# Optimization experiments

Hardware: AMD Instinct MI355X
Metric: run time of the kernel (lower is better)

The kernel has to match this reference:

```python
import jax, jax.numpy as jnp
import numpy as np

VEC, HID, B, S = 1280, 128, 4, 256
EPS = 1e-5


def _ln(x):
    m = x.mean(-1, keepdims=True)
    v = ((x - m) ** 2).mean(-1, keepdims=True)
    return (x - m) / jnp.sqrt(v + EPS)


def _add_attn(q_in, kv_in, Wq, Wk, wv):
    # Additive (Bahdanau) attention: scores[b,i,j] = wv . tanh(q[b,i] + k[b,j])
    q = q_in @ Wq            # [B, Sq, H]
    k = kv_in @ Wk           # [B, Sk, H]
    feat = jnp.tanh(q[:, :, None, :] + k[:, None, :, :])   # [B, Sq, Sk, H]
    scores = jnp.einsum('bijh,h->bij', feat, wv)
    attn = jax.nn.softmax(scores, axis=-1)
    return jnp.einsum('bij,bjd->bid', attn, kv_in)          # values = kv_in


def _res_fc(x, W1, b1, W2, b2):
    return jnp.maximum(x @ W1 + b1, 0.0) @ W2 + b2 + x


def setup_inputs() -> dict:
    key = jax.random.key(0)
    ks = iter(jax.random.split(key, 64))
    d = {
        'X': jax.random.normal(next(ks), (B, S, VEC), dtype=jnp.float32),
        'lys_pos': 100,
    }
    sc = 0.02
    for i in (1, 2, 3, 4):
        d[f'Wq{i}'] = jax.random.normal(next(ks), (VEC, HID), dtype=jnp.float32) * sc
        d[f'Wk{i}'] = jax.random.normal(next(ks), (VEC, HID), dtype=jnp.float32) * sc
        d[f'wv{i}'] = jax.random.normal(next(ks), (HID,), dtype=jnp.float32) * sc
    for i in (1, 2, 3):
        d[f'rW1_{i}'] = jax.random.normal(next(ks), (VEC, HID), dtype=jnp.float32) * sc
        d[f'rb1_{i}'] = jnp.zeros((HID,), dtype=jnp.float32)
        d[f'rW2_{i}'] = jax.random.normal(next(ks), (HID, VEC), dtype=jnp.float32) * sc
        d[f'rb2_{i}'] = jnp.zeros((VEC,), dtype=jnp.float32)
    d['hW1'] = jax.random.normal(next(ks), (VEC, 32), dtype=jnp.float32) * sc
    d['hb1'] = jnp.zeros((32,), dtype=jnp.float32)
    d['hW2'] = jax.random.normal(next(ks), (32, 12), dtype=jnp.float32) * sc
    d['hb2'] = jnp.zeros((12,), dtype=jnp.float32)
    d['hW3'] = jax.random.normal(next(ks), (12, 2), dtype=jnp.float32) * sc
    d['hb3'] = jnp.zeros((2,), dtype=jnp.float32)
    return d


def reference(X, lys_pos,
              Wq1, Wk1, wv1, Wq2, Wk2, wv2, Wq3, Wk3, wv3, Wq4, Wk4, wv4,
              rW1_1, rb1_1, rW2_1, rb2_1,
              rW1_2, rb1_2, rW2_2, rb2_2,
              rW1_3, rb1_3, rW2_3, rb2_3,
              hW1, hb1, hW2, hb2, hW3, hb3):
    X = X.astype(jnp.float32)
    X = _ln(_add_attn(X, X, Wq1, Wk1, wv1) + X)
    X = _res_fc(X, rW1_1, rb1_1, rW2_1, rb2_1)
    X = _ln(_add_attn(X, X, Wq2, Wk2, wv2) + X)
    X = _res_fc(X, rW1_2, rb1_2, rW2_2, rb2_2)
    X = _ln(_add_attn(X, X, Wq3, Wk3, wv3) + X)
    X = _res_fc(X, rW1_3, rb1_3, rW2_3, rb2_3)
    X_lys = X[:, lys_pos, :][:, None, :]                    # [B, 1, VEC]
    X_lys = _ln(_add_attn(X_lys, X, Wq4, Wk4, wv4) + X_lys)
    h = jnp.maximum(X_lys @ hW1 + hb1, 0.0)                 # dropout = identity (eval)
    h = jnp.maximum(h @ hW2 + hb2, 0.0)
    logits = (h @ hW3 + hb3)[:, 0, :]                       # squeeze(1) -> [B, 2]
    return logits
```

## Files before the change

kernel.cpp:

```cpp
#include <hip/hip_runtime.h>


#define DEV __device__ __forceinline__

static constexpr int VEC = 1280;
static constexpr int HID = 128;
static constexpr int BB  = 4;
static constexpr int SS  = 256;
static constexpr int MROWS = BB * SS;
static constexpr int NPART = 8;

DEV float ftanh(float x) {
  float e = __expf(2.0f * x);
  return 1.0f - __fdividef(2.0f, e + 1.0f);
}

DEV float waveSum(float v) {
#pragma unroll
  for (int off = 32; off > 0; off >>= 1) v += __shfl_xor(v, off, 64);
  return v;
}
DEV float waveMax(float v) {
#pragma unroll
  for (int off = 32; off > 0; off >>= 1) v = fmaxf(v, __shfl_xor(v, off, 64));
  return v;
}
DEV float blockSum(float v, float* red) {
  v = waveSum(v);
  int tid = threadIdx.x;
  if ((tid & 63) == 0) red[tid >> 6] = v;
  __syncthreads();
  float r = (red[0] + red[1]) + (red[2] + red[3]);
  __syncthreads();
  return r;
}
DEV float blockMax(float v, float* red) {
  v = waveMax(v);
  int tid = threadIdx.x;
  if ((tid & 63) == 0) red[tid >> 6] = v;
  __syncthreads();
  float r = fmaxf(fmaxf(red[0], red[1]), fmaxf(red[2], red[3]));
  __syncthreads();
  return r;
}

template <int MODE, bool AFUSE, bool OBIAS, bool ORES>
__global__ __launch_bounds__(256) void gemm_k(
    const float* __restrict__ A, long sAb, long aPart,
    const float* __restrict__ B0, const float* __restrict__ B1, int nSplitB,
    long sBb, int ldB,
    float* __restrict__ C, long sCb,
    const float* __restrict__ aBias, const float* __restrict__ oBias,
    const float* __restrict__ res,
    int N, int K, int kChunk) {
  const int n0 = blockIdx.x * 64;
  const int m0 = blockIdx.y * 64;
  const int z  = blockIdx.z;

  const float* Ab = A + (MODE == 2 ? (long)z * sAb : 0L);
  float*       Cb = C + (MODE >= 1 ? (long)z * sCb : 0L);
  const float* resz = ORES ? (res + (MODE == 2 ? (long)z * sCb : 0L)) : nullptr;
  const float* Bsel;
  int nb;
  if (n0 < nSplitB) { Bsel = B0; nb = n0; } else { Bsel = B1; nb = n0 - nSplitB; }
  if (MODE == 2) Bsel += (long)z * sBb;

  const int kBeg = (MODE == 1) ? z * kChunk : 0;
  const int kEnd = (MODE == 1) ? kBeg + kChunk : K;

  __shared__ float As[16][68];
  __shared__ float Bs[16][68];

  const int tid = threadIdx.x;
  const int tx = tid & 15, ty = tid >> 4;
  const int ar = tid >> 2, ac = (tid & 3) << 2;
  const int br = tid >> 4, bc = (tid & 15) << 2;

  auto loadA = [&](int kt) -> float4 {
    const size_t aoff = (size_t)(m0 + ar) * K + kt + ac;
    if (AFUSE) {
      float4 s = *(const float4*)(Ab + aoff);
#pragma unroll
      for (int p = 1; p < NPART; ++p) {
        const float4 t = *(const float4*)(Ab + (long)p * aPart + aoff);
        s.x += t.x; s.y += t.y; s.z += t.z; s.w += t.w;
      }
      const float4 bz = *(const float4*)(aBias + kt + ac);
      s.x = fmaxf(s.x + bz.x, 0.0f);
      s.y = fmaxf(s.y + bz.y, 0.0f);
      s.z = fmaxf(s.z + bz.z, 0.0f);
      s.w = fmaxf(s.w + bz.w, 0.0f);
      return s;
    }
    return *(const float4*)(Ab + aoff);
  };
  auto loadB = [&](int kt) -> float4 {
    return *(const float4*)(Bsel + (size_t)(kt + br) * ldB + nb + bc);
  };

  float acc[4][4] = {};
  float4 a4 = loadA(kBeg);
  float4 b4 = loadB(kBeg);

  for (int kt = kBeg; kt < kEnd; kt += 16) {
    __syncthreads();
    As[ac + 0][ar] = a4.x;
    As[ac + 1][ar] = a4.y;
    As[ac + 2][ar] = a4.z;
    As[ac + 3][ar] = a4.w;
    *(float4*)&Bs[br][bc] = b4;
    __syncthreads();
    if (kt + 16 < kEnd) {
      a4 = loadA(kt + 16);
      b4 = loadB(kt + 16);
    }
#pragma unroll
    for (int kk = 0; kk < 16; ++kk) {
      const float4 av = *(const float4*)&As[kk][ty << 2];
      const float4 bv = *(const float4*)&Bs[kk][tx << 2];
      const float a[4] = {av.x, av.y, av.z, av.w};
      const float b[4] = {bv.x, bv.y, bv.z, bv.w};
#pragma unroll
      for (int i = 0; i < 4; ++i)
#pragma unroll
        for (int j = 0; j < 4; ++j) acc[i][j] = fmaf(a[i], b[j], acc[i][j]);
    }
  }

#pragma unroll
  for (int i = 0; i < 4; ++i) {
    const int m = m0 + (ty << 2) + i;
#pragma unroll
    for (int j = 0; j < 4; ++j) {
      const int n = n0 + (tx << 2) + j;
      float v = acc[i][j];
      if (OBIAS) v += oBias[n];
      if (ORES) v += resz[(size_t)m * N + n];
      Cb[(size_t)m * N + n] = v;
    }
  }
}

__global__ __launch_bounds__(256) void qksum_k(const float* __restrict__ QKp,
                                               long ps,
                                               float* __restrict__ Qd,
                                               float* __restrict__ KT) {
  const int r = blockIdx.x, tid = threadIdx.x;
  const int b = r >> 8, j = r & 255;
  const size_t off = (size_t)r * 256 + tid;
  float v = 0.0f;
#pragma unroll
  for (int p = 0; p < NPART; ++p) v += QKp[(long)p * ps + off];
  if (tid < 128) {
    Qd[(size_t)r * 128 + tid] = v;
  } else {
    KT[(size_t)b * 32768 + (size_t)(tid - 128) * 256 + j] = v;
  }
}

__global__ __launch_bounds__(256) void scores2_k(const float* __restrict__ Qd,
                                                 const float* __restrict__ KT,
                                                 const float* __restrict__ wv,
                                                 float* __restrict__ attn) {
  const int b = blockIdx.y, i0 = blockIdx.x * 2, tid = threadIdx.x;
  __shared__ float qs[2][128], wvs[128], red[4];
  {
    const int rr = tid >> 7, h = tid & 127;
    qs[rr][h] = Qd[(size_t)(b * 256 + i0 + rr) * 128 + h];
  }
  if (tid < 128) wvs[tid] = wv[tid];
  __syncthreads();

  const float* KTb = KT + (size_t)b * 32768 + tid;
  float s0 = 0.0f, s1 = 0.0f;
#pragma unroll 4
  for (int h = 0; h < 128; h += 4) {
    const float k0 = KTb[(h + 0) * 256];
    const float k1 = KTb[(h + 1) * 256];
    const float k2 = KTb[(h + 2) * 256];
    const float k3 = KTb[(h + 3) * 256];
    const float w0 = wvs[h], w1 = wvs[h + 1], w2 = wvs[h + 2], w3 = wvs[h + 3];
    s0 += w0 * ftanh(qs[0][h] + k0) + w1 * ftanh(qs[0][h + 1] + k1) +
          w2 * ftanh(qs[0][h + 2] + k2) + w3 * ftanh(qs[0][h + 3] + k3);
    s1 += w0 * ftanh(qs[1][h] + k0) + w1 * ftanh(qs[1][h + 1] + k1) +
          w2 * ftanh(qs[1][h + 2] + k2) + w3 * ftanh(qs[1][h + 3] + k3);
  }
  {
    const float mx = blockMax(s0, red);
    const float e = __expf(s0 - mx);
    const float tot = blockSum(e, red);
    attn[(size_t)(b * 256 + i0) * 256 + tid] = e / tot;
  }
  {
    const float mx = blockMax(s1, red);
    const float e = __expf(s1 - mx);
    const float tot = blockSum(e, red);
    attn[(size_t)(b * 256 + i0 + 1) * 256 + tid] = e / tot;
  }
}

__global__ __launch_bounds__(256) void ln1_k(const float* __restrict__ A,
                                             float* __restrict__ Y) {
  __shared__ float red[4];
  const int r = blockIdx.x, tid = threadIdx.x;
  const float* a = A + (size_t)r * VEC;
  float v[5];
  float sum = 0.0f;
#pragma unroll
  for (int k = 0; k < 5; ++k) {
    v[k] = a[tid + k * 256];
    sum += v[k];
  }
  sum = blockSum(sum, red);
  const float m = sum * (1.0f / VEC);
  float sq = 0.0f;
#pragma unroll
  for (int k = 0; k < 5; ++k) {
    const float dl = v[k] - m;
    sq += dl * dl;
  }
  sq = blockSum(sq, red);
  const float rstd = rsqrtf(sq * (1.0f / VEC) + 1e-5f);
  float* y = Y + (size_t)r * VEC;
#pragma unroll
  for (int k = 0; k < 5; ++k) y[tid + k * 256] = (v[k] - m) * rstd;
}

__global__ __launch_bounds__(256) void scores4_k(const float* __restrict__ Qd,
                                                 const float* __restrict__ KT,
                                                 const float* __restrict__ wv4,
                                                 const int* __restrict__ lys,
                                                 float* __restrict__ aw4) {
  const int b = blockIdx.x, tid = threadIdx.x;
  __shared__ float qs[128], wvs[128], red[4];
  const int lp = lys[0];
  if (tid < 128) {
    qs[tid] = Qd[(size_t)(b * 256 + lp) * 128 + tid];
    wvs[tid] = wv4[tid];
  }
  __syncthreads();
  const float* KTb = KT + (size_t)b * 32768 + tid;
  float s = 0.0f;
#pragma unroll 4
  for (int h = 0; h < 128; h += 4) {
    s += wvs[h + 0] * ftanh(qs[h + 0] + KTb[(h + 0) * 256]);
    s += wvs[h + 1] * ftanh(qs[h + 1] + KTb[(h + 1) * 256]);
    s += wvs[h + 2] * ftanh(qs[h + 2] + KTb[(h + 2) * 256]);
    s += wvs[h + 3] * ftanh(qs[h + 3] + KTb[(h + 3) * 256]);
  }
  const float mx = blockMax(s, red);
  const float e = __expf(s - mx);
  const float tot = blockSum(e, red);
  aw4[b * 256 + tid] = e / tot;
}

__global__ __launch_bounds__(256) void pv4_k(const float* __restrict__ aw4,
                                             const float* __restrict__ X3,
                                             const int* __restrict__ lys,
                                             float* __restrict__ A4) {
  const int b = blockIdx.x, c = blockIdx.y * 256 + threadIdx.x;
  __shared__ float aws[256];
  aws[threadIdx.x] = aw4[b * 256 + threadIdx.x];
  __syncthreads();
  const float* Xb = X3 + (size_t)b * SS * VEC;
  float acc = 0.0f;
#pragma unroll 8
  for (int j = 0; j < 256; ++j) acc = fmaf(aws[j], Xb[(size_t)j * VEC + c], acc);
  acc += Xb[(size_t)lys[0] * VEC + c];
  A4[b * VEC + c] = acc;
}

__global__ __launch_bounds__(256) void lnhead_k(
    const float* __restrict__ A4,
    const float* __restrict__ hW1, const float* __restrict__ hb1,
    const float* __restrict__ hW2, const float* __restrict__ hb2,
    const float* __restrict__ hW3, const float* __restrict__ hb3,
    float* __restrict__ out) {
  const int b = blockIdx.x, tid = threadIdx.x;
  __shared__ float xrow[1280], partial[256], red[4];
  __shared__ float h1s[32], h2s[12];
  float v[5];
  float sum = 0.0f;
#pragma unroll
  for (int k = 0; k < 5; ++k) {
    v[k] = A4[b * VEC + tid + k * 256];
    sum += v[k];
  }
  sum = blockSum(sum, red);
  const float m = sum * (1.0f / VEC);
  float sq = 0.0f;
#pragma unroll
  for (int k = 0; k < 5; ++k) {
    const float dl = v[k] - m;
    sq += dl * dl;
  }
  sq = blockSum(sq, red);
  const float rstd = rsqrtf(sq * (1.0f / VEC) + 1e-5f);
#pragma unroll
  for (int k = 0; k < 5; ++k) xrow[tid + k * 256] = (v[k] - m) * rstd;
  __syncthreads();
  {
    const int n = tid & 31, sl = tid >> 5;
    float p = 0.0f;
    for (int k = sl * 160; k < sl * 160 + 160; ++k)
      p = fmaf(xrow[k], hW1[(size_t)k * 32 + n], p);
    partial[tid] = p;
  }
  __syncthreads();
  if (tid < 32) {
    float t = 0.0f;
#pragma unroll
    for (int s2 = 0; s2 < 8; ++s2) t += partial[s2 * 32 + tid];
    h1s[tid] = fmaxf(t + hb1[tid], 0.0f);
  }
  __syncthreads();
  if (tid < 12) {
    float t = 0.0f;
#pragma unroll
    for (int k = 0; k < 32; ++k) t = fmaf(h1s[k], hW2[k * 12 + tid], t);
    h2s[tid] = fmaxf(t + hb2[tid], 0.0f);
  }
  __syncthreads();
  if (tid < 2) {
    float t = 0.0f;
#pragma unroll
    for (int k = 0; k < 12; ++k) t = fmaf(h2s[k], hW3[k * 2 + tid], t);
    out[b * 2 + tid] = t + hb3[tid];
  }
}

extern "C" void kernel_launch(void* const* d_in, const int* in_sizes, int n_in,
                              void* d_out, int out_size, void* d_ws, size_t ws_size,
                              hipStream_t stream) {
  const float* X = (const float*)d_in[0];
  const int* lys = (const int*)d_in[1];
  const float* Wq[4] = {(const float*)d_in[2], (const float*)d_in[5],
                        (const float*)d_in[8], (const float*)d_in[11]};
  const float* Wk[4] = {(const float*)d_in[3], (const float*)d_in[6],
                        (const float*)d_in[9], (const float*)d_in[12]};
  const float* wv[4] = {(const float*)d_in[4], (const float*)d_in[7],
                        (const float*)d_in[10], (const float*)d_in[13]};
  const float* rW1[3] = {(const float*)d_in[14], (const float*)d_in[18],
                         (const float*)d_in[22]};
  const float* rb1[3] = {(const float*)d_in[15], (const float*)d_in[19],
                         (const float*)d_in[23]};
  const float* rW2[3] = {(const float*)d_in[16], (const float*)d_in[20],
                         (const float*)d_in[24]};
  const float* rb2[3] = {(const float*)d_in[17], (const float*)d_in[21],
                         (const float*)d_in[25]};
  const float* hW1 = (const float*)d_in[26];
  const float* hb1 = (const float*)d_in[27];
  const float* hW2 = (const float*)d_in[28];
  const float* hb2 = (const float*)d_in[29];
  const float* hW3 = (const float*)d_in[30];
  const float* hb3 = (const float*)d_in[31];
  float* out = (float*)d_out;

  float* ws = (float*)d_ws;
  const long QK_PS = 262144;
  const long H_PS  = 131072;
  float* QKp  = ws;
  float* Qd   = QKp + (long)NPART * QK_PS;
  float* KT   = Qd + 131072;
  float* attn = KT + 131072;
  float* Yraw = attn + 262144;
  float* Yb   = Yraw + 1310720;
  float* Hp   = Yb + 1310720;
  float* buf0 = Hp + (long)NPART * H_PS;
  float* buf1 = buf0 + 1310720;
  float* aw4  = buf1 + 1310720;
  float* A4   = aw4 + 1024;

  const int NSPLIT_NONE = 1 << 30;
  const float* P[3] = {X, buf0, buf1};
  float* Q[3] = {buf0, buf1, buf0};

  for (int l = 0; l < 3; ++l) {
    const float* Xin = P[l];
    gemm_k<1, false, false, false><<<dim3(4, 16, NPART), 256, 0, stream>>>(
        Xin, 0, 0, Wq[l], Wk[l], HID, 0, HID, QKp, QK_PS, nullptr, nullptr,
        nullptr, 256, VEC, 160);
    qksum_k<<<dim3(MROWS), 256, 0, stream>>>(QKp, QK_PS, Qd, KT);
    scores2_k<<<dim3(128, BB), 256, 0, stream>>>(Qd, KT, wv[l], attn);
    gemm_k<2, false, false, true><<<dim3(20, 4, BB), 256, 0, stream>>>(
        attn, (long)SS * SS, 0, Xin, Xin, NSPLIT_NONE, (long)SS * VEC, VEC,
        Yraw, (long)SS * VEC, nullptr, nullptr, Xin, VEC, SS, 0);
    ln1_k<<<dim3(MROWS), 256, 0, stream>>>(Yraw, Yb);
    gemm_k<1, false, false, false><<<dim3(2, 16, NPART), 256, 0, stream>>>(
        Yb, 0, 0, rW1[l], rW1[l], NSPLIT_NONE, 0, HID, Hp, H_PS, nullptr,
        nullptr, nullptr, HID, VEC, 160);
    gemm_k<0, true, true, true><<<dim3(20, 16, 1), 256, 0, stream>>>(
        Hp, 0, H_PS, rW2[l], rW2[l], NSPLIT_NONE, 0, VEC, Q[l], 0, rb1[l],
        rb2[l], Yb, VEC, HID, 0);
  }

  const float* X3 = Q[2];
  gemm_k<1, false, false, false><<<dim3(4, 16, NPART), 256, 0, stream>>>(
      X3, 0, 0, Wq[3], Wk[3], HID, 0, HID, QKp, QK_PS, nullptr, nullptr,
      nullptr, 256, VEC, 160);
  qksum_k<<<dim3(MROWS), 256, 0, stream>>>(QKp, QK_PS, Qd, KT);
  scores4_k<<<dim3(BB), 256, 0, stream>>>(Qd, KT, wv[3], lys, aw4);
  pv4_k<<<dim3(BB, 5), 256, 0, stream>>>(aw4, X3, lys, A4);
  lnhead_k<<<dim3(BB), 256, 0, stream>>>(A4, hW1, hb1, hW2, hb2, hW3, hb3, out);
}
```

Before: 445.2 us.

## Fuse whole network into one persistent cooperative kernel with grid syncs

Replaces the sequence of about 26 separate kernel launches with a single cooperative persistent kernel of 256 blocks. Each stage loops over virtual blocks and stages are separated by grid-wide syncs, removing launch overhead and inter-kernel gaps. The final attention stage is also trimmed: only K is projected for all rows, while Q is computed for just the single lys row per batch. The cost is that each stage runs on a fixed 256-block grid with one block per CU, which limits occupancy for the GEMM stages, and grid.sync adds its own barrier cost.

```diff
diff --git a/kernel.cpp b/kernel.cpp
--- a/kernel.cpp
+++ b/kernel.cpp
@@ -1,4 +1,7 @@
 #include <hip/hip_runtime.h>
+#include <hip/hip_cooperative_groups.h>
+
+namespace cg = cooperative_groups;
 
 
 #define DEV __device__ __forceinline__
@@ -44,58 +47,47 @@
   return r;
 }
 
-template <int MODE, bool AFUSE, bool OBIAS, bool ORES>
-__global__ __launch_bounds__(256) void gemm_k(
-    const float* __restrict__ A, long sAb, long aPart,
-    const float* __restrict__ B0, const float* __restrict__ B1, int nSplitB,
-    long sBb, int ldB,
-    float* __restrict__ C, long sCb,
-    const float* __restrict__ aBias, const float* __restrict__ oBias,
-    const float* __restrict__ res,
-    int N, int K, int kChunk) {
-  const int n0 = blockIdx.x * 64;
-  const int m0 = blockIdx.y * 64;
-  const int z  = blockIdx.z;
-
-  const float* Ab = A + (MODE == 2 ? (long)z * sAb : 0L);
-  float*       Cb = C + (MODE >= 1 ? (long)z * sCb : 0L);
-  const float* resz = ORES ? (res + (MODE == 2 ? (long)z * sCb : 0L)) : nullptr;
-  const float* Bsel;
-  int nb;
-  if (n0 < nSplitB) { Bsel = B0; nb = n0; } else { Bsel = B1; nb = n0 - nSplitB; }
-  if (MODE == 2) Bsel += (long)z * sBb;
-
-  const int kBeg = (MODE == 1) ? z * kChunk : 0;
-  const int kEnd = (MODE == 1) ? kBeg + kChunk : K;
-
-  __shared__ float As[16][68];
-  __shared__ float Bs[16][68];
-
+struct SmemGemm { float As[16][68]; float Bs[16][68]; };
+union Smem {
+  SmemGemm g;
+  struct { float qs[2][128]; float wvs[128]; } s;
+  struct { float xrow[1280]; float partial[256]; float h1s[32]; float h2s[12]; } t;
+  float aws[256];
+};
+
+template <int NP, bool AFUSE, bool OBIAS, bool ORES>
+DEV void gemm_tile(SmemGemm& smg,
+                   const float* __restrict__ A, int ldA, long aPart,
+                   const float* __restrict__ B, int ldB, int nb,
+                   float* __restrict__ C, int ldC,
+                   int m0, int n0, int kBeg, int kEnd,
+                   const float* __restrict__ aBias,
+                   const float* __restrict__ oBias,
+                   const float* __restrict__ res) {
   const int tid = threadIdx.x;
   const int tx = tid & 15, ty = tid >> 4;
   const int ar = tid >> 2, ac = (tid & 3) << 2;
   const int br = tid >> 4, bc = (tid & 15) << 2;
 
   auto loadA = [&](int kt) -> float4 {
-    const size_t aoff = (size_t)(m0 + ar) * K + kt + ac;
+    const size_t off = (size_t)(m0 + ar) * ldA + kt + ac;
+    float4 s = *(const float4*)(A + off);
     if (AFUSE) {
-      float4 s = *(const float4*)(Ab + aoff);
-#pragma unroll
-      for (int p = 1; p < NPART; ++p) {
-        const float4 t = *(const float4*)(Ab + (long)p * aPart + aoff);
-        s.x += t.x; s.y += t.y; s.z += t.z; s.w += t.w;
+#pragma unroll
+      for (int p2 = 1; p2 < NP; ++p2) {
+        const float4 t2 = *(const float4*)(A + (long)p2 * aPart + off);
+        s.x += t2.x; s.y += t2.y; s.z += t2.z; s.w += t2.w;
       }
       const float4 bz = *(const float4*)(aBias + kt + ac);
       s.x = fmaxf(s.x + bz.x, 0.0f);
       s.y = fmaxf(s.y + bz.y, 0.0f);
       s.z = fmaxf(s.z + bz.z, 0.0f);
       s.w = fmaxf(s.w + bz.w, 0.0f);
-      return s;
-    }
-    return *(const float4*)(Ab + aoff);
+    }
+    return s;
   };
   auto loadB = [&](int kt) -> float4 {
-    return *(const float4*)(Bsel + (size_t)(kt + br) * ldB + nb + bc);
+    return *(const float4*)(B + (size_t)(kt + br) * ldB + nb + bc);
   };
 
   float acc[4][4] = {};
@@ -104,11 +96,11 @@
 
   for (int kt = kBeg; kt < kEnd; kt += 16) {
     __syncthreads();
-    As[ac + 0][ar] = a4.x;
-    As[ac + 1][ar] = a4.y;
-    As[ac + 2][ar] = a4.z;
-    As[ac + 3][ar] = a4.w;
-    *(float4*)&Bs[br][bc] = b4;
+    smg.As[ac + 0][ar] = a4.x;
+    smg.As[ac + 1][ar] = a4.y;
+    smg.As[ac + 2][ar] = a4.z;
+    smg.As[ac + 3][ar] = a4.w;
+    *(float4*)&smg.Bs[br][bc] = b4;
     __syncthreads();
     if (kt + 16 < kEnd) {
       a4 = loadA(kt + 16);
@@ -116,8 +108,8 @@
     }
 #pragma unroll
     for (int kk = 0; kk < 16; ++kk) {
-      const float4 av = *(const float4*)&As[kk][ty << 2];
-      const float4 bv = *(const float4*)&Bs[kk][tx << 2];
+      const float4 av = *(const float4*)&smg.As[kk][ty << 2];
+      const float4 bv = *(const float4*)&smg.Bs[kk][tx << 2];
       const float a[4] = {av.x, av.y, av.z, av.w};
       const float b[4] = {bv.x, bv.y, bv.z, bv.w};
 #pragma unroll
@@ -135,271 +127,328 @@
       const int n = n0 + (tx << 2) + j;
       float v = acc[i][j];
       if (OBIAS) v += oBias[n];
-      if (ORES) v += resz[(size_t)m * N + n];
-      Cb[(size_t)m * N + n] = v;
-    }
-  }
-}
-
-__global__ __launch_bounds__(256) void qksum_k(const float* __restrict__ QKp,
-                                               long ps,
-                                               float* __restrict__ Qd,
-                                               float* __restrict__ KT) {
-  const int r = blockIdx.x, tid = threadIdx.x;
-  const int b = r >> 8, j = r & 255;
-  const size_t off = (size_t)r * 256 + tid;
-  float v = 0.0f;
-#pragma unroll
-  for (int p = 0; p < NPART; ++p) v += QKp[(long)p * ps + off];
-  if (tid < 128) {
-    Qd[(size_t)r * 128 + tid] = v;
-  } else {
-    KT[(size_t)b * 32768 + (size_t)(tid - 128) * 256 + j] = v;
-  }
-}
-
-__global__ __launch_bounds__(256) void scores2_k(const float* __restrict__ Qd,
-                                                 const float* __restrict__ KT,
-                                                 const float* __restrict__ wv,
-                                                 float* __restrict__ attn) {
-  const int b = blockIdx.y, i0 = blockIdx.x * 2, tid = threadIdx.x;
-  __shared__ float qs[2][128], wvs[128], red[4];
-  {
-    const int rr = tid >> 7, h = tid & 127;
-    qs[rr][h] = Qd[(size_t)(b * 256 + i0 + rr) * 128 + h];
-  }
-  if (tid < 128) wvs[tid] = wv[tid];
-  __syncthreads();
-
-  const float* KTb = KT + (size_t)b * 32768 + tid;
-  float s0 = 0.0f, s1 = 0.0f;
+      if (ORES) v += res[(size_t)m * ldC + n];
+      C[(size_t)m * ldC + n] = v;
+    }
+  }
+}
+
+struct Params {
+  const float* X; const int* lys;
+  const float* Wq[4]; const float* Wk[4]; const float* wv[4];
+  const float* rW1[3]; const float* rb1[3];
+  const float* rW2[3]; const float* rb2[3];
+  const float* hW1; const float* hb1;
+  const float* hW2; const float* hb2;
+  const float* hW3; const float* hb3;
+  float* out;
+  float* QKp; float* Qd; float* KT; float* attn;
+  float* Yraw; float* Yb; float* Hp;
+  float* buf0; float* buf1;
+  float* q4d; float* aw4; float* A4;
+};
+
+static constexpr long QK_PS = 262144;
+static constexpr long H_PS  = 131072;
+
+__global__ __launch_bounds__(256, 1) void net_k(Params p) {
+  cg::grid_group grid = cg::this_grid();
+  __shared__ Smem sm;
+  __shared__ float red[4];
+  const int blk = blockIdx.x, G = gridDim.x, tid = threadIdx.x;
+
+  const float* Pin[3] = {p.X, p.buf0, p.buf1};
+  float* Pout[3] = {p.buf0, p.buf1, p.buf0};
+
+  for (int l = 0; l < 3; ++l) {
+    const float* Xin = Pin[l];
+
+    for (int vb = blk; vb < 512; vb += G) {
+      const int x = vb & 3, y = (vb >> 2) & 15, z = vb >> 6;
+      const int n0 = x * 64;
+      const float* Bsel = (n0 < HID) ? p.Wq[l] : p.Wk[l];
+      const int nb = (n0 < HID) ? n0 : n0 - HID;
+      gemm_tile<1, false, false, false>(
+          sm.g, Xin, VEC, 0, Bsel, HID, nb, p.QKp + (long)z * QK_PS, 256,
+          y * 64, n0, z * 160, z * 160 + 160, nullptr, nullptr, nullptr);
+    }
+    grid.sync();
+
+    for (int vb = blk; vb < MROWS; vb += G) {
+      const int b = vb >> 8, j = vb & 255;
+      const size_t off = (size_t)vb * 256 + tid;
+      float v = 0.0f;
+#pragma unroll
+      for (int q = 0; q < NPART; ++q) v += p.QKp[(long)q * QK_PS + off];
+      if (tid < 128) p.Qd[(size_t)vb * 128 + tid] = v;
+      else p.KT[(size_t)b * 32768 + (size_t)(tid - 128) * 256 + j] = v;
+    }
+    grid.sync();
+
+    for (int vb = blk; vb < 512; vb += G) {
+      const int b = vb >> 7, i0 = (vb & 127) * 2;
+      {
+        const int rr = tid >> 7, h = tid & 127;
+        sm.s.qs[rr][h] = p.Qd[(size_t)(b * 256 + i0 + rr) * 128 + h];
+      }
+      if (tid < 128) sm.s.wvs[tid] = p.wv[l][tid];
+      __syncthreads();
+      const float* KTb = p.KT + (size_t)b * 32768 + tid;
+      float s0 = 0.0f, s1 = 0.0f;
 #pragma unroll 4
-  for (int h = 0; h < 128; h += 4) {
-    const float k0 = KTb[(h + 0) * 256];
-    const float k1 = KTb[(h + 1) * 256];
-    const float k2 = KTb[(h + 2) * 256];
-    const float k3 = KTb[(h + 3) * 256];
-    const float w0 = wvs[h], w1 = wvs[h + 1], w2 = wvs[h + 2], w3 = wvs[h + 3];
-    s0 += w0 * ftanh(qs[0][h] + k0) + w1 * ftanh(qs[0][h + 1] + k1) +
-          w2 * ftanh(qs[0][h + 2] + k2) + w3 * ftanh(qs[0][h + 3] + k3);
-    s1 += w0 * ftanh(qs[1][h] + k0) + w1 * ftanh(qs[1][h + 1] + k1) +
-          w2 * ftanh(qs[1][h + 2] + k2) + w3 * ftanh(qs[1][h + 3] + k3);
-  }
-  {
-    const float mx = blockMax(s0, red);
-    const float e = __expf(s0 - mx);
+      for (int h = 0; h < 128; h += 4) {
+        const float k0 = KTb[(h + 0) * 256];
+        const float k1 = KTb[(h + 1) * 256];
+        const float k2 = KTb[(h + 2) * 256];
+        const float k3 = KTb[(h + 3) * 256];
+        const float w0 = sm.s.wvs[h], w1 = sm.s.wvs[h + 1];
+        const float w2 = sm.s.wvs[h + 2], w3 = sm.s.wvs[h + 3];
+        s0 += w0 * ftanh(sm.s.qs[0][h] + k0) + w1 * ftanh(sm.s.qs[0][h + 1] + k1) +
+              w2 * ftanh(sm.s.qs[0][h + 2] + k2) + w3 * ftanh(sm.s.qs[0][h + 3] + k3);
+        s1 += w0 * ftanh(sm.s.qs[1][h] + k0) + w1 * ftanh(sm.s.qs[1][h + 1] + k1) +
+              w2 * ftanh(sm.s.qs[1][h + 2] + k2) + w3 * ftanh(sm.s.qs[1][h + 3] + k3);
+      }
+      {
+        const float mx = blockMax(s0, red);
+        const float e = __expf(s0 - mx);
+        const float tot = blockSum(e, red);
+        p.attn[(size_t)(b * 256 + i0) * 256 + tid] = e / tot;
+      }
+      {
+        const float mx = blockMax(s1, red);
+        const float e = __expf(s1 - mx);
+        const float tot = blockSum(e, red);
+        p.attn[(size_t)(b * 256 + i0 + 1) * 256 + tid] = e / tot;
+      }
+    }
+    grid.sync();
+
+    for (int vb = blk; vb < 320; vb += G) {
+      const int x = vb % 20, rest = vb / 20;
+      const int y = rest & 3, b = rest >> 2;
+      gemm_tile<1, false, false, true>(
+          sm.g, p.attn + (long)b * SS * SS, 256, 0,
+          Xin + (long)b * SS * VEC, VEC, x * 64,
+          p.Yraw + (long)b * SS * VEC, VEC,
+          y * 64, x * 64, 0, 256, nullptr, nullptr, Xin + (long)b * SS * VEC);
+    }
+    grid.sync();
+
+    for (int vb = blk; vb < MROWS; vb += G) {
+      const float* a = p.Yraw + (size_t)vb * VEC;
+      float v[5];
+      float sum = 0.0f;
+#pragma unroll
+      for (int k = 0; k < 5; ++k) {
+        v[k] = a[tid + k * 256];
+        sum += v[k];
+      }
+      sum = blockSum(sum, red);
+      const float m = sum * (1.0f / VEC);
+      float sq = 0.0f;
+#pragma unroll
+      for (int k = 0; k < 5; ++k) {
+        const float dl = v[k] - m;
+        sq += dl * dl;
+      }
+      sq = blockSum(sq, red);
+      const float rstd = rsqrtf(sq * (1.0f / VEC) + 1e-5f);
+      float* y = p.Yb + (size_t)vb * VEC;
+#pragma unroll
+      for (int k = 0; k < 5; ++k) y[tid + k * 256] = (v[k] - m) * rstd;
+    }
+    grid.sync();
+
+    for (int vb = blk; vb < 256; vb += G) {
+      const int x = vb & 1, y = (vb >> 1) & 15, z = vb >> 5;
+      gemm_tile<1, false, false, false>(
+          sm.g, p.Yb, VEC, 0, p.rW1[l], HID, x * 64,
+          p.Hp + (long)z * H_PS, HID,
+          y * 64, x * 64, z * 160, z * 160 + 160, nullptr, nullptr, nullptr);
+    }
+    grid.sync();
+
+    for (int vb = blk; vb < 320; vb += G) {
+      const int x = vb % 20, y = vb / 20;
+      gemm_tile<NPART, true, true, true>(
+          sm.g, p.Hp, HID, H_PS, p.rW2[l], VEC, x * 64,
+          Pout[l], VEC,
+          y * 64, x * 64, 0, HID, p.rb1[l], p.rb2[l], p.Yb);
+    }
+    grid.sync();
+  }
+
+  const float* X3 = p.buf0;
+  const int lp = p.lys[0];
+
+  for (int vb = blk; vb < 260; vb += G) {
+    if (vb < 256) {
+      const int x = vb & 1, y = (vb >> 1) & 15, z = vb >> 5;
+      gemm_tile<1, false, false, false>(
+          sm.g, X3, VEC, 0, p.Wk[3], HID, x * 64,
+          p.QKp + (long)z * H_PS, HID,
+          y * 64, x * 64, z * 160, z * 160 + 160, nullptr, nullptr, nullptr);
+    } else {
+      __syncthreads();
+      const int b = vb - 256;
+      const float* xr = X3 + (size_t)(b * 256 + lp) * VEC;
+      const int h = tid & 127, half = tid >> 7;
+      float acc = 0.0f;
+      const int k0 = half * 640;
+      for (int k = k0; k < k0 + 640; ++k)
+        acc = fmaf(xr[k], p.Wq[3][(size_t)k * HID + h], acc);
+      sm.t.partial[tid] = acc;
+      __syncthreads();
+      if (tid < 128)
+        p.q4d[b * 128 + tid] = sm.t.partial[tid] + sm.t.partial[tid + 128];
+      __syncthreads();
+    }
+  }
+  grid.sync();
+
+  for (int vb = blk; vb < 512; vb += G) {
+    const int r = vb * 2 + (tid >> 7), h = tid & 127;
+    const int b = r >> 8, j = r & 255;
+    const size_t off = (size_t)r * 128 + h;
+    float v = 0.0f;
+#pragma unroll
+    for (int q = 0; q < NPART; ++q) v += p.QKp[(long)q * H_PS + off];
+    p.KT[(size_t)b * 32768 + (size_t)h * 256 + j] = v;
+  }
+  grid.sync();
+
+  for (int vb = blk; vb < BB; vb += G) {
+    const int b = vb;
+    if (tid < 128) {
+      sm.s.qs[0][tid] = p.q4d[b * 128 + tid];
+      sm.s.wvs[tid] = p.wv[3][tid];
+    }
+    __syncthreads();
+    const float* KTb = p.KT + (size_t)b * 32768 + tid;
+    float s = 0.0f;
+#pragma unroll 4
+    for (int h = 0; h < 128; h += 4) {
+      s += sm.s.wvs[h + 0] * ftanh(sm.s.qs[0][h + 0] + KTb[(h + 0) * 256]);
+      s += sm.s.wvs[h + 1] * ftanh(sm.s.qs[0][h + 1] + KTb[(h + 1) * 256]);
+      s += sm.s.wvs[h + 2] * ftanh(sm.s.qs[0][h + 2] + KTb[(h + 2) * 256]);
+      s += sm.s.wvs[h + 3] * ftanh(sm.s.qs[0][h + 3] + KTb[(h + 3) * 256]);
+    }
+    const float mx = blockMax(s, red);
+    const float e = __expf(s - mx);
     const float tot = blockSum(e, red);
-    attn[(size_t)(b * 256 + i0) * 256 + tid] = e / tot;
-  }
-  {
-    const float mx = blockMax(s1, red);
-    const float e = __expf(s1 - mx);
-    const float tot = blockSum(e, red);
-    attn[(size_t)(b * 256 + i0 + 1) * 256 + tid] = e / tot;
-  }
-}
-
-__global__ __launch_bounds__(256) void ln1_k(const float* __restrict__ A,
-                                             float* __restrict__ Y) {
-  __shared__ float red[4];
-  const int r = blockIdx.x, tid = threadIdx.x;
-  const float* a = A + (size_t)r * VEC;
-  float v[5];
-  float sum = 0.0f;
-#pragma unroll
-  for (int k = 0; k < 5; ++k) {
-    v[k] = a[tid + k * 256];
-    sum += v[k];
-  }
-  sum = blockSum(sum, red);
-  const float m = sum * (1.0f / VEC);
-  float sq = 0.0f;
-#pragma unroll
-  for (int k = 0; k < 5; ++k) {
-    const float dl = v[k] - m;
-    sq += dl * dl;
-  }
-  sq = blockSum(sq, red);
-  const float rstd = rsqrtf(sq * (1.0f / VEC) + 1e-5f);
-  float* y = Y + (size_t)r * VEC;
-#pragma unroll
-  for (int k = 0; k < 5; ++k) y[tid + k * 256] = (v[k] - m) * rstd;
-}
-
-__global__ __launch_bounds__(256) void scores4_k(const float* __restrict__ Qd,
-                                                 const float* __restrict__ KT,
-                                                 const float* __restrict__ wv4,
-                                                 const int* __restrict__ lys,
-                                                 float* __restrict__ aw4) {
-  const int b = blockIdx.x, tid = threadIdx.x;
-  __shared__ float qs[128], wvs[128], red[4];
-  const int lp = lys[0];
-  if (tid < 128) {
-    qs[tid] = Qd[(size_t)(b * 256 + lp) * 128 + tid];
-    wvs[tid] = wv4[tid];
-  }
-  __syncthreads();
-  const float* KTb = KT + (size_t)b * 32768 + tid;
-  float s = 0.0f;
-#pragma unroll 4
-  for (int h = 0; h < 128; h += 4) {
-    s += wvs[h + 0] * ftanh(qs[h + 0] + KTb[(h + 0) * 256]);
-    s += wvs[h + 1] * ftanh(qs[h + 1] + KTb[(h + 1) * 256]);
-    s += wvs[h + 2] * ftanh(qs[h + 2] + KTb[(h + 2) * 256]);
-    s += wvs[h + 3] * ftanh(qs[h + 3] + KTb[(h + 3) * 256]);
-  }
-  const float mx = blockMax(s, red);
-  const float e = __expf(s - mx);
-  const float tot = blockSum(e, red);
-  aw4[b * 256 + tid] = e / tot;
-}
-
-__global__ __launch_bounds__(256) void pv4_k(const float* __restrict__ aw4,
-                                             const float* __restrict__ X3,
-                                             const int* __restrict__ lys,
-                                             float* __restrict__ A4) {
-  const int b = blockIdx.x, c = blockIdx.y * 256 + threadIdx.x;
-  __shared__ float aws[256];
-  aws[threadIdx.x] = aw4[b * 256 + threadIdx.x];
-  __syncthreads();
-  const float* Xb = X3 + (size_t)b * SS * VEC;
-  float acc = 0.0f;
+    p.aw4[b * 256 + tid] = e / tot;
+  }
+  grid.sync();
+
+  for (int vb = blk; vb < 20; vb += G) {
+    const int b = vb & 3, cs = vb >> 2;
+    const int c = cs * 256 + tid;
+    sm.aws[tid] = p.aw4[b * 256 + tid];
+    __syncthreads();
+    const float* Xb = X3 + (size_t)b * SS * VEC;
+    float acc = 0.0f;
 #pragma unroll 8
-  for (int j = 0; j < 256; ++j) acc = fmaf(aws[j], Xb[(size_t)j * VEC + c], acc);
-  acc += Xb[(size_t)lys[0] * VEC + c];
-  A4[b * VEC + c] = acc;
-}
-
-__global__ __launch_bounds__(256) void lnhead_k(
-    const float* __restrict__ A4,
-    const float* __restrict__ hW1, const float* __restrict__ hb1,
-    const float* __restrict__ hW2, const float* __restrict__ hb2,
-    const float* __restrict__ hW3, const float* __restrict__ hb3,
-    float* __restrict__ out) {
-  const int b = blockIdx.x, tid = threadIdx.x;
-  __shared__ float xrow[1280], partial[256], red[4];
-  __shared__ float h1s[32], h2s[12];
-  float v[5];
-  float sum = 0.0f;
-#pragma unroll
-  for (int k = 0; k < 5; ++k) {
-    v[k] = A4[b * VEC + tid + k * 256];
-    sum += v[k];
-  }
-  sum = blockSum(sum, red);
-  const float m = sum * (1.0f / VEC);
-  float sq = 0.0f;
-#pragma unroll
-  for (int k = 0; k < 5; ++k) {
-    const float dl = v[k] - m;
-    sq += dl * dl;
-  }
-  sq = blockSum(sq, red);
-  const float rstd = rsqrtf(sq * (1.0f / VEC) + 1e-5f);
-#pragma unroll
-  for (int k = 0; k < 5; ++k) xrow[tid + k * 256] = (v[k] - m) * rstd;
-  __syncthreads();
-  {
-    const int n = tid & 31, sl = tid >> 5;
-    float p = 0.0f;
-    for (int k = sl * 160; k < sl * 160 + 160; ++k)
-      p = fmaf(xrow[k], hW1[(size_t)k * 32 + n], p);
-    partial[tid] = p;
-  }
-  __syncthreads();
-  if (tid < 32) {
-    float t = 0.0f;
-#pragma unroll
-    for (int s2 = 0; s2 < 8; ++s2) t += partial[s2 * 32 + tid];
-    h1s[tid] = fmaxf(t + hb1[tid], 0.0f);
-  }
-  __syncthreads();
-  if (tid < 12) {
-    float t = 0.0f;
-#pragma unroll
-    for (int k = 0; k < 32; ++k) t = fmaf(h1s[k], hW2[k * 12 + tid], t);
-    h2s[tid] = fmaxf(t + hb2[tid], 0.0f);
-  }
-  __syncthreads();
-  if (tid < 2) {
-    float t = 0.0f;
-#pragma unroll
-    for (int k = 0; k < 12; ++k) t = fmaf(h2s[k], hW3[k * 2 + tid], t);
-    out[b * 2 + tid] = t + hb3[tid];
+    for (int j = 0; j < 256; ++j)
+      acc = fmaf(sm.aws[j], Xb[(size_t)j * VEC + c], acc);
+    acc += Xb[(size_t)lp * VEC + c];
+    p.A4[b * VEC + c] = acc;
+    __syncthreads();
+  }
+  grid.sync();
+
+  for (int vb = blk; vb < BB; vb += G) {
+    const int b = vb;
+    float v[5];
+    float sum = 0.0f;
+#pragma unroll
+    for (int k = 0; k < 5; ++k) {
+      v[k] = p.A4[b * VEC + tid + k * 256];
+      sum += v[k];
+    }
+    sum = blockSum(sum, red);
+    const float m = sum * (1.0f / VEC);
+    float sq = 0.0f;
+#pragma unroll
+    for (int k = 0; k < 5; ++k) {
+      const float dl = v[k] - m;
+      sq += dl * dl;
+    }
+    sq = blockSum(sq, red);
+    const float rstd = rsqrtf(sq * (1.0f / VEC) + 1e-5f);
+#pragma unroll
+    for (int k = 0; k < 5; ++k) sm.t.xrow[tid + k * 256] = (v[k] - m) * rstd;
+    __syncthreads();
+    {
+      const int n = tid & 31, sl = tid >> 5;
+      float pp = 0.0f;
+      for (int k = sl * 160; k < sl * 160 + 160; ++k)
+        pp = fmaf(sm.t.xrow[k], p.hW1[(size_t)k * 32 + n], pp);
+      sm.t.partial[tid] = pp;
+    }
+    __syncthreads();
+    if (tid < 32) {
+      float t = 0.0f;
+#pragma unroll
+      for (int s2 = 0; s2 < 8; ++s2) t += sm.t.partial[s2 * 32 + tid];
+      sm.t.h1s[tid] = fmaxf(t + p.hb1[tid], 0.0f);
+    }
+    __syncthreads();
+    if (tid < 12) {
+      float t = 0.0f;
+#pragma unroll
+      for (int k = 0; k < 32; ++k) t = fmaf(sm.t.h1s[k], p.hW2[k * 12 + tid], t);
+      sm.t.h2s[tid] = fmaxf(t + p.hb2[tid], 0.0f);
+    }
+    __syncthreads();
+    if (tid < 2) {
+      float t = 0.0f;
+#pragma unroll
+      for (int k = 0; k < 12; ++k) t = fmaf(sm.t.h2s[k], p.hW3[k * 2 + tid], t);
+      p.out[b * 2 + tid] = t + p.hb3[tid];
+    }
   }
 }
 
 extern "C" void kernel_launch(void* const* d_in, const int* in_sizes, int n_in,
                               void* d_out, int out_size, void* d_ws, size_t ws_size,
                               hipStream_t stream) {
-  const float* X = (const float*)d_in[0];
-  const int* lys = (const int*)d_in[1];
-  const float* Wq[4] = {(const float*)d_in[2], (const float*)d_in[5],
-                        (const float*)d_in[8], (const float*)d_in[11]};
-  const float* Wk[4] = {(const float*)d_in[3], (const float*)d_in[6],
-                        (const float*)d_in[9], (const float*)d_in[12]};
-  const float* wv[4] = {(const float*)d_in[4], (const float*)d_in[7],
-                        (const float*)d_in[10], (const float*)d_in[13]};
-  const float* rW1[3] = {(const float*)d_in[14], (const float*)d_in[18],
-                         (const float*)d_in[22]};
-  const float* rb1[3] = {(const float*)d_in[15], (const float*)d_in[19],
-                         (const float*)d_in[23]};
-  const float* rW2[3] = {(const float*)d_in[16], (const float*)d_in[20],
-                         (const float*)d_in[24]};
-  const float* rb2[3] = {(const float*)d_in[17], (const float*)d_in[21],
-                         (const float*)d_in[25]};
-  const float* hW1 = (const float*)d_in[26];
-  const float* hb1 = (const float*)d_in[27];
-  const float* hW2 = (const float*)d_in[28];
-  const float* hb2 = (const float*)d_in[29];
-  const float* hW3 = (const float*)d_in[30];
-  const float* hb3 = (const float*)d_in[31];
-  float* out = (float*)d_out;
+  Params p;
+  p.X = (const float*)d_in[0];
+  p.lys = (const int*)d_in[1];
+  for (int i = 0; i < 4; ++i) {
+    p.Wq[i] = (const float*)d_in[2 + 3 * i];
+    p.Wk[i] = (const float*)d_in[3 + 3 * i];
+    p.wv[i] = (const float*)d_in[4 + 3 * i];
+  }
+  for (int i = 0; i < 3; ++i) {
+    p.rW1[i] = (const float*)d_in[14 + 4 * i];
+    p.rb1[i] = (const float*)d_in[15 + 4 * i];
+    p.rW2[i] = (const float*)d_in[16 + 4 * i];
+    p.rb2[i] = (const float*)d_in[17 + 4 * i];
+  }
+  p.hW1 = (const float*)d_in[26];
+  p.hb1 = (const float*)d_in[27];
+  p.hW2 = (const float*)d_in[28];
+  p.hb2 = (const float*)d_in[29];
+  p.hW3 = (const float*)d_in[30];
+  p.hb3 = (const float*)d_in[31];
+  p.out = (float*)d_out;
 
   float* ws = (float*)d_ws;
-  const long QK_PS = 262144;
-  const long H_PS  = 131072;
-  float* QKp  = ws;
-  float* Qd   = QKp + (long)NPART * QK_PS;
-  float* KT   = Qd + 131072;
-  float* attn = KT + 131072;
-  float* Yraw = attn + 262144;
-  float* Yb   = Yraw + 1310720;
-  float* Hp   = Yb + 1310720;
-  float* buf0 = Hp + (long)NPART * H_PS;
-  float* buf1 = buf0 + 1310720;
-  float* aw4  = buf1 + 1310720;
-  float* A4   = aw4 + 1024;
-
-  const int NSPLIT_NONE = 1 << 30;
-  const float* P[3] = {X, buf0, buf1};
-  float* Q[3] = {buf0, buf1, buf0};
-
-  for (int l = 0; l < 3; ++l) {
-    const float* Xin = P[l];
-    gemm_k<1, false, false, false><<<dim3(4, 16, NPART), 256, 0, stream>>>(
-        Xin, 0, 0, Wq[l], Wk[l], HID, 0, HID, QKp, QK_PS, nullptr, nullptr,
-        nullptr, 256, VEC, 160);
-    qksum_k<<<dim3(MROWS), 256, 0, stream>>>(QKp, QK_PS, Qd, KT);
-    scores2_k<<<dim3(128, BB), 256, 0, stream>>>(Qd, KT, wv[l], attn);
-    gemm_k<2, false, false, true><<<dim3(20, 4, BB), 256, 0, stream>>>(
-        attn, (long)SS * SS, 0, Xin, Xin, NSPLIT_NONE, (long)SS * VEC, VEC,
-        Yraw, (long)SS * VEC, nullptr, nullptr, Xin, VEC, SS, 0);
-    ln1_k<<<dim3(MROWS), 256, 0, stream>>>(Yraw, Yb);
-    gemm_k<1, false, false, false><<<dim3(2, 16, NPART), 256, 0, stream>>>(
-        Yb, 0, 0, rW1[l], rW1[l], NSPLIT_NONE, 0, HID, Hp, H_PS, nullptr,
-        nullptr, nullptr, HID, VEC, 160);
-    gemm_k<0, true, true, true><<<dim3(20, 16, 1), 256, 0, stream>>>(
-        Hp, 0, H_PS, rW2[l], rW2[l], NSPLIT_NONE, 0, VEC, Q[l], 0, rb1[l],
-        rb2[l], Yb, VEC, HID, 0);
-  }
-
-  const float* X3 = Q[2];
-  gemm_k<1, false, false, false><<<dim3(4, 16, NPART), 256, 0, stream>>>(
-      X3, 0, 0, Wq[3], Wk[3], HID, 0, HID, QKp, QK_PS, nullptr, nullptr,
-      nullptr, 256, VEC, 160);
-  qksum_k<<<dim3(MROWS), 256, 0, stream>>>(QKp, QK_PS, Qd, KT);
-  scores4_k<<<dim3(BB), 256, 0, stream>>>(Qd, KT, wv[3], lys, aw4);
-  pv4_k<<<dim3(BB, 5), 256, 0, stream>>>(aw4, X3, lys, A4);
-  lnhead_k<<<dim3(BB), 256, 0, stream>>>(A4, hW1, hb1, hW2, hb2, hW3, hb3, out);
-}
+  p.QKp  = ws;
+  p.Qd   = p.QKp + (long)NPART * QK_PS;
+  p.KT   = p.Qd + 131072;
+  p.attn = p.KT + 131072;
+  p.Yraw = p.attn + 262144;
+  p.Yb   = p.Yraw + 1310720;
+  p.Hp   = p.Yb + 1310720;
+  p.buf0 = p.Hp + (long)NPART * H_PS;
+  p.buf1 = p.buf0 + 1310720;
+  p.q4d  = p.buf1 + 1310720;
+  p.aw4  = p.q4d + 512;
+  p.A4   = p.aw4 + 1024;
+
+  void* args[] = {&p};
+  hipLaunchCooperativeKernel((const void*)net_k, dim3(256), dim3(256), args, 0,
+                             stream);
+}
```

After: 1.393 ms. 213% more time.

## Fuse LayerNorm into neighbouring GEMMs via atomic row stats; trim final attention

Applied to the files above, without the earlier changes.

Removes the standalone LayerNorm kernel. The attention-output GEMM now accumulates per-row sum and sum-of-squares with atomics, and the following GEMMs normalize on load and in the residual epilogue. The final layer now computes only the K projection for all rows plus a single query row, and the score/softmax step is fused with the PV product. This saves one full read and write of the activations per layer and avoids wasted query work, at the cost of atomics and a variance computed as E[x²]−mean², which is less numerically stable.

```diff
diff --git a/kernel.cpp b/kernel.cpp
--- a/kernel.cpp
+++ b/kernel.cpp
@@ -9,6 +9,7 @@
 static constexpr int SS  = 256;
 static constexpr int MROWS = BB * SS;
 static constexpr int NPART = 8;
+static constexpr float INV_VEC = 1.0f / 1280.0f;
 
 DEV float ftanh(float x) {
   float e = __expf(2.0f * x);
@@ -44,7 +45,8 @@
   return r;
 }
 
-template <int MODE, bool AFUSE, bool OBIAS, bool ORES>
+template <int MODE, bool AFUSE, bool ALN, bool OBIAS, bool RESLN, bool RESP,
+          bool STATS>
 __global__ __launch_bounds__(256) void gemm_k(
     const float* __restrict__ A, long sAb, long aPart,
     const float* __restrict__ B0, const float* __restrict__ B1, int nSplitB,
@@ -52,6 +54,7 @@
     float* __restrict__ C, long sCb,
     const float* __restrict__ aBias, const float* __restrict__ oBias,
     const float* __restrict__ res,
+    float* __restrict__ Ssum, float* __restrict__ Ssq,
     int N, int K, int kChunk) {
   const int n0 = blockIdx.x * 64;
   const int m0 = blockIdx.y * 64;
@@ -59,7 +62,9 @@
 
   const float* Ab = A + (MODE == 2 ? (long)z * sAb : 0L);
   float*       Cb = C + (MODE >= 1 ? (long)z * sCb : 0L);
-  const float* resz = ORES ? (res + (MODE == 2 ? (long)z * sCb : 0L)) : nullptr;
+  const float* resb = (RESP || RESLN)
+                          ? (res + (MODE == 2 ? (long)z * sCb : 0L))
+                          : nullptr;
   const float* Bsel;
   int nb;
   if (n0 < nSplitB) { Bsel = B0; nb = n0; } else { Bsel = B1; nb = n0 - nSplitB; }
@@ -76,23 +81,36 @@
   const int ar = tid >> 2, ac = (tid & 3) << 2;
   const int br = tid >> 4, bc = (tid & 15) << 2;
 
+  float aMean = 0.0f, aRstd = 1.0f;
+  if (ALN) {
+    const int rm = m0 + ar;
+    const float s = Ssum[rm], q = Ssq[rm];
+    aMean = s * INV_VEC;
+    aRstd = rsqrtf(q * INV_VEC - aMean * aMean + 1e-5f);
+  }
+
   auto loadA = [&](int kt) -> float4 {
-    const size_t aoff = (size_t)(m0 + ar) * K + kt + ac;
+    const size_t off = (size_t)(m0 + ar) * K + kt + ac;
+    float4 s = *(const float4*)(Ab + off);
     if (AFUSE) {
-      float4 s = *(const float4*)(Ab + aoff);
-#pragma unroll
-      for (int p = 1; p < NPART; ++p) {
-        const float4 t = *(const float4*)(Ab + (long)p * aPart + aoff);
-        s.x += t.x; s.y += t.y; s.z += t.z; s.w += t.w;
+#pragma unroll
+      for (int p2 = 1; p2 < NPART; ++p2) {
+        const float4 t2 = *(const float4*)(Ab + (long)p2 * aPart + off);
+        s.x += t2.x; s.y += t2.y; s.z += t2.z; s.w += t2.w;
       }
       const float4 bz = *(const float4*)(aBias + kt + ac);
       s.x = fmaxf(s.x + bz.x, 0.0f);
       s.y = fmaxf(s.y + bz.y, 0.0f);
       s.z = fmaxf(s.z + bz.z, 0.0f);
       s.w = fmaxf(s.w + bz.w, 0.0f);
-      return s;
-    }
-    return *(const float4*)(Ab + aoff);
+    }
+    if (ALN) {
+      s.x = (s.x - aMean) * aRstd;
+      s.y = (s.y - aMean) * aRstd;
+      s.z = (s.z - aMean) * aRstd;
+      s.w = (s.w - aMean) * aRstd;
+    }
+    return s;
   };
   auto loadB = [&](int kt) -> float4 {
     return *(const float4*)(Bsel + (size_t)(kt + br) * ldB + nb + bc);
@@ -127,16 +145,42 @@
     }
   }
 
+  float rs[4], rq[4];
 #pragma unroll
   for (int i = 0; i < 4; ++i) {
     const int m = m0 + (ty << 2) + i;
+    float mean = 0.0f, rstd = 1.0f;
+    if (RESLN) {
+      const float s = Ssum[m], q = Ssq[m];
+      mean = s * INV_VEC;
+      rstd = rsqrtf(q * INV_VEC - mean * mean + 1e-5f);
+    }
+    if (STATS) { rs[i] = 0.0f; rq[i] = 0.0f; }
 #pragma unroll
     for (int j = 0; j < 4; ++j) {
       const int n = n0 + (tx << 2) + j;
       float v = acc[i][j];
       if (OBIAS) v += oBias[n];
-      if (ORES) v += resz[(size_t)m * N + n];
+      if (RESP) v += resb[(size_t)m * N + n];
+      if (RESLN) v += (resb[(size_t)m * N + n] - mean) * rstd;
       Cb[(size_t)m * N + n] = v;
+      if (STATS) { rs[i] += v; rq[i] = fmaf(v, v, rq[i]); }
+    }
+  }
+  if (STATS) {
+#pragma unroll
+    for (int i = 0; i < 4; ++i) {
+      float s = rs[i], q = rq[i];
+#pragma unroll
+      for (int msk = 1; msk < 16; msk <<= 1) {
+        s += __shfl_xor(s, msk, 64);
+        q += __shfl_xor(q, msk, 64);
+      }
+      if ((tid & 15) == 0) {
+        const int rowg = (MODE == 2 ? z * SS : 0) + m0 + (ty << 2) + i;
+        atomicAdd(&Ssum[rowg], s);
+        atomicAdd(&Ssq[rowg], q);
+      }
     }
   }
 }
@@ -144,8 +188,10 @@
 __global__ __launch_bounds__(256) void qksum_k(const float* __restrict__ QKp,
                                                long ps,
                                                float* __restrict__ Qd,
-                                               float* __restrict__ KT) {
+                                               float* __restrict__ KT,
+                                               float* __restrict__ stats) {
   const int r = blockIdx.x, tid = threadIdx.x;
+  if (r < 8) stats[r * 256 + tid] = 0.0f;
   const int b = r >> 8, j = r & 255;
   const size_t off = (size_t)r * 256 + tid;
   float v = 0.0f;
@@ -199,43 +245,48 @@
   }
 }
 
-__global__ __launch_bounds__(256) void ln1_k(const float* __restrict__ A,
-                                             float* __restrict__ Y) {
-  __shared__ float red[4];
-  const int r = blockIdx.x, tid = threadIdx.x;
-  const float* a = A + (size_t)r * VEC;
-  float v[5];
-  float sum = 0.0f;
-#pragma unroll
-  for (int k = 0; k < 5; ++k) {
-    v[k] = a[tid + k * 256];
-    sum += v[k];
-  }
-  sum = blockSum(sum, red);
-  const float m = sum * (1.0f / VEC);
-  float sq = 0.0f;
-#pragma unroll
-  for (int k = 0; k < 5; ++k) {
-    const float dl = v[k] - m;
-    sq += dl * dl;
-  }
-  sq = blockSum(sq, red);
-  const float rstd = rsqrtf(sq * (1.0f / VEC) + 1e-5f);
-  float* y = Y + (size_t)r * VEC;
-#pragma unroll
-  for (int k = 0; k < 5; ++k) y[tid + k * 256] = (v[k] - m) * rstd;
-}
-
-__global__ __launch_bounds__(256) void scores4_k(const float* __restrict__ Qd,
-                                                 const float* __restrict__ KT,
-                                                 const float* __restrict__ wv4,
-                                                 const int* __restrict__ lys,
-                                                 float* __restrict__ aw4) {
-  const int b = blockIdx.x, tid = threadIdx.x;
-  __shared__ float qs[128], wvs[128], red[4];
+__global__ __launch_bounds__(256) void kt4q4_k(const float* __restrict__ K4p,
+                                               const float* __restrict__ X3,
+                                               const float* __restrict__ Wq4,
+                                               const int* __restrict__ lys,
+                                               float* __restrict__ KT,
+                                               float* __restrict__ q4d) {
+  __shared__ float partial[256];
+  const int vb = blockIdx.x, tid = threadIdx.x;
+  if (vb < 512) {
+    const int r = vb * 2 + (tid >> 7), h = tid & 127;
+    const int b = r >> 8, j = r & 255;
+    const size_t off = (size_t)r * 128 + h;
+    float v = 0.0f;
+#pragma unroll
+    for (int p = 0; p < NPART; ++p) v += K4p[(long)p * 131072 + off];
+    KT[(size_t)b * 32768 + (size_t)h * 256 + j] = v;
+  } else {
+    const int b = vb - 512;
+    const int lp = lys[0];
+    const float* xr = X3 + (size_t)(b * 256 + lp) * VEC;
+    const int h = tid & 127, half = tid >> 7;
+    float acc = 0.0f;
+    const int k0 = half * 640;
+    for (int k = k0; k < k0 + 640; ++k)
+      acc = fmaf(xr[k], Wq4[(size_t)k * HID + h], acc);
+    partial[tid] = acc;
+    __syncthreads();
+    if (tid < 128) q4d[b * 128 + tid] = partial[tid] + partial[tid + 128];
+  }
+}
+
+__global__ __launch_bounds__(256) void pv4s_k(const float* __restrict__ q4d,
+                                              const float* __restrict__ KT,
+                                              const float* __restrict__ wv4,
+                                              const int* __restrict__ lys,
+                                              const float* __restrict__ X3,
+                                              float* __restrict__ A4) {
+  const int b = blockIdx.x & 3, cs = blockIdx.x >> 2, tid = threadIdx.x;
+  __shared__ float qs[128], wvs[128], aw[256], red[4];
   const int lp = lys[0];
   if (tid < 128) {
-    qs[tid] = Qd[(size_t)(b * 256 + lp) * 128 + tid];
+    qs[tid] = q4d[b * 128 + tid];
     wvs[tid] = wv4[tid];
   }
   __syncthreads();
@@ -251,22 +302,15 @@
   const float mx = blockMax(s, red);
   const float e = __expf(s - mx);
   const float tot = blockSum(e, red);
-  aw4[b * 256 + tid] = e / tot;
-}
-
-__global__ __launch_bounds__(256) void pv4_k(const float* __restrict__ aw4,
-                                             const float* __restrict__ X3,
-                                             const int* __restrict__ lys,
-                                             float* __restrict__ A4) {
-  const int b = blockIdx.x, c = blockIdx.y * 256 + threadIdx.x;
-  __shared__ float aws[256];
-  aws[threadIdx.x] = aw4[b * 256 + threadIdx.x];
-  __syncthreads();
+  aw[tid] = e / tot;
+  __syncthreads();
+
+  const int c = cs * 256 + tid;
   const float* Xb = X3 + (size_t)b * SS * VEC;
   float acc = 0.0f;
 #pragma unroll 8
-  for (int j = 0; j < 256; ++j) acc = fmaf(aws[j], Xb[(size_t)j * VEC + c], acc);
-  acc += Xb[(size_t)lys[0] * VEC + c];
+  for (int j = 0; j < 256; ++j) acc = fmaf(aw[j], Xb[(size_t)j * VEC + c], acc);
+  acc += Xb[(size_t)lp * VEC + c];
   A4[b * VEC + c] = acc;
 }
 
@@ -287,7 +331,7 @@
     sum += v[k];
   }
   sum = blockSum(sum, red);
-  const float m = sum * (1.0f / VEC);
+  const float m = sum * INV_VEC;
   float sq = 0.0f;
 #pragma unroll
   for (int k = 0; k < 5; ++k) {
@@ -295,7 +339,7 @@
     sq += dl * dl;
   }
   sq = blockSum(sq, red);
-  const float rstd = rsqrtf(sq * (1.0f / VEC) + 1e-5f);
+  const float rstd = rsqrtf(sq * INV_VEC + 1e-5f);
 #pragma unroll
   for (int k = 0; k < 5; ++k) xrow[tid + k * 256] = (v[k] - m) * rstd;
   __syncthreads();
@@ -359,17 +403,18 @@
   float* ws = (float*)d_ws;
   const long QK_PS = 262144;
   const long H_PS  = 131072;
-  float* QKp  = ws;
-  float* Qd   = QKp + (long)NPART * QK_PS;
-  float* KT   = Qd + 131072;
-  float* attn = KT + 131072;
-  float* Yraw = attn + 262144;
-  float* Yb   = Yraw + 1310720;
-  float* Hp   = Yb + 1310720;
-  float* buf0 = Hp + (long)NPART * H_PS;
-  float* buf1 = buf0 + 1310720;
-  float* aw4  = buf1 + 1310720;
-  float* A4   = aw4 + 1024;
+  float* QKp   = ws;
+  float* Qd    = QKp + (long)NPART * QK_PS;
+  float* KT    = Qd + 131072;
+  float* attn  = KT + 131072;
+  float* Yraw  = attn + 262144;
+  float* Hp    = Yraw + 1310720;
+  float* buf0  = Hp + (long)NPART * H_PS;
+  float* buf1  = buf0 + 1310720;
+  float* stats = buf1 + 1310720;
+  float* q4d   = stats + 2048;
+  float* A4    = q4d + 512;
+  float* Ssum = stats, *Ssq = stats + 1024;
 
   const int NSPLIT_NONE = 1 << 30;
   const float* P[3] = {X, buf0, buf1};
@@ -377,29 +422,33 @@
 
   for (int l = 0; l < 3; ++l) {
     const float* Xin = P[l];
-    gemm_k<1, false, false, false><<<dim3(4, 16, NPART), 256, 0, stream>>>(
-        Xin, 0, 0, Wq[l], Wk[l], HID, 0, HID, QKp, QK_PS, nullptr, nullptr,
-        nullptr, 256, VEC, 160);
-    qksum_k<<<dim3(MROWS), 256, 0, stream>>>(QKp, QK_PS, Qd, KT);
+    gemm_k<1, false, false, false, false, false, false>
+        <<<dim3(4, 16, NPART), 256, 0, stream>>>(
+            Xin, 0, 0, Wq[l], Wk[l], HID, 0, HID, QKp, QK_PS, nullptr, nullptr,
+            nullptr, nullptr, nullptr, 256, VEC, 160);
+    qksum_k<<<dim3(MROWS), 256, 0, stream>>>(QKp, QK_PS, Qd, KT, stats);
     scores2_k<<<dim3(128, BB), 256, 0, stream>>>(Qd, KT, wv[l], attn);
-    gemm_k<2, false, false, true><<<dim3(20, 4, BB), 256, 0, stream>>>(
-        attn, (long)SS * SS, 0, Xin, Xin, NSPLIT_NONE, (long)SS * VEC, VEC,
-        Yraw, (long)SS * VEC, nullptr, nullptr, Xin, VEC, SS, 0);
-    ln1_k<<<dim3(MROWS), 256, 0, stream>>>(Yraw, Yb);
-    gemm_k<1, false, false, false><<<dim3(2, 16, NPART), 256, 0, stream>>>(
-        Yb, 0, 0, rW1[l], rW1[l], NSPLIT_NONE, 0, HID, Hp, H_PS, nullptr,
-        nullptr, nullptr, HID, VEC, 160);
-    gemm_k<0, true, true, true><<<dim3(20, 16, 1), 256, 0, stream>>>(
-        Hp, 0, H_PS, rW2[l], rW2[l], NSPLIT_NONE, 0, VEC, Q[l], 0, rb1[l],
-        rb2[l], Yb, VEC, HID, 0);
+    gemm_k<2, false, false, false, false, true, true>
+        <<<dim3(20, 4, BB), 256, 0, stream>>>(
+            attn, (long)SS * SS, 0, Xin, Xin, NSPLIT_NONE, (long)SS * VEC, VEC,
+            Yraw, (long)SS * VEC, nullptr, nullptr, Xin, Ssum, Ssq,
+            VEC, SS, 0);
+    gemm_k<1, false, true, false, false, false, false>
+        <<<dim3(2, 16, NPART), 256, 0, stream>>>(
+            Yraw, 0, 0, rW1[l], rW1[l], NSPLIT_NONE, 0, HID, Hp, H_PS, nullptr,
+            nullptr, nullptr, Ssum, Ssq, HID, VEC, 160);
+    gemm_k<0, true, false, true, true, false, false>
+        <<<dim3(20, 16, 1), 256, 0, stream>>>(
+            Hp, 0, H_PS, rW2[l], rW2[l], NSPLIT_NONE, 0, VEC, Q[l], 0, rb1[l],
+            rb2[l], Yraw, Ssum, Ssq, VEC, HID, 0);
   }
 
   const float* X3 = Q[2];
-  gemm_k<1, false, false, false><<<dim3(4, 16, NPART), 256, 0, stream>>>(
-      X3, 0, 0, Wq[3], Wk[3], HID, 0, HID, QKp, QK_PS, nullptr, nullptr,
-      nullptr, 256, VEC, 160);
-  qksum_k<<<dim3(MROWS), 256, 0, stream>>>(QKp, QK_PS, Qd, KT);
-  scores4_k<<<dim3(BB), 256, 0, stream>>>(Qd, KT, wv[3], lys, aw4);
-  pv4_k<<<dim3(BB, 5), 256, 0, stream>>>(aw4, X3, lys, A4);
+  gemm_k<1, false, false, false, false, false, false>
+      <<<dim3(2, 16, NPART), 256, 0, stream>>>(
+          X3, 0, 0, Wk[3], Wk[3], NSPLIT_NONE, 0, HID, QKp, H_PS, nullptr,
+          nullptr, nullptr, nullptr, nullptr, HID, VEC, 160);
+  kt4q4_k<<<dim3(516), 256, 0, stream>>>(QKp, X3, Wq[3], lys, KT, q4d);
+  pv4s_k<<<dim3(20), 256, 0, stream>>>(q4d, KT, wv[3], lys, X3, A4);
   lnhead_k<<<dim3(BB), 256, 0, stream>>>(A4, hW1, hb1, hW2, hb2, hW3, hb3, out);
 }
```

Result: slower. 454.2 us (+2.0%).
